# Kernel optimization log

Measured on AMD Instinct MI355X. Metric: run time of the kernel, lower is better.

The kernel has to match this reference:

```python
import jax, jax.numpy as jnp
import numpy as np

N_NODES = 100000   # graph size N
DIM     = 128      # embedding dim d
M_SEL   = 4096     # selected nodes per forward
N_POS   = 32       # positives per node (padded/fixed sample of pos_neigh)
N_NEG   = 256      # negatives per node (fixed sample of neg_samples)


def setup_inputs() -> dict:
    key = jax.random.key(0)
    ks = jax.random.split(key, 8)
    return {
        "P": jax.random.normal(ks[0], (N_NODES, DIM), dtype=jnp.float32),
        "W_d": jax.random.normal(ks[1], (DIM,), dtype=jnp.float32),
        "deg_vec": jax.random.uniform(ks[2], (N_NODES,), dtype=jnp.float32) * 64.0,
        "nodes": jax.random.randint(ks[3], (M_SEL,), 0, N_NODES),
        "pos_idx": jax.random.randint(ks[4], (M_SEL, N_POS), 0, N_NODES),
        "neg_idx": jax.random.randint(ks[5], (M_SEL, N_NEG), 0, N_NODES),
        "deg_pos_idx": jax.random.randint(ks[6], (M_SEL, N_POS), 0, N_NODES),
        "deg_neg_idx": jax.random.randint(ks[7], (M_SEL, N_NEG), 0, N_NODES),
    }


def my_sigmoid(x):
    # Sigmoid_alt: sign-carrying sigmoid in (-1, 1) (parity used in the repo's plots)
    return 2.0 * jax.nn.sigmoid(x) - 1.0


def _contrast(Z, nodes, pos_idx, neg_idx):
    # softmax_formula vectorized over the selected-node batch:
    #   loss_i = -( mean_p hamming(Z_i, Z_p) - log sum_n exp(hamming(Z_i, Z_n)) )
    Zi = Z[nodes]                                            # [M, d]
    h_pos = jnp.abs(Zi[:, None, :] - Z[pos_idx]).sum(-1)    # [M, P]
    h_neg = jnp.abs(Zi[:, None, :] - Z[neg_idx]).sum(-1)    # [M, K]
    log_sum_neg = jax.scipy.special.logsumexp(h_neg, axis=1)  # stable log(sum(exp(.)))
    per_node = log_sum_neg - h_pos.mean(axis=1)
    return per_node.sum()


def reference(P, W_d, deg_vec, nodes, pos_idx, neg_idx, deg_pos_idx, deg_neg_idx):
    Z = my_sigmoid(P)                                        # [N, d]
    # degree_loss: MSE(Z @ W_d, deg_vec)
    L_deg = jnp.mean((Z @ W_d - deg_vec) ** 2)
    # contrast_adj_n_degDist: adjacency and degree-distribution contrastive totals
    L_adj = _contrast(Z, nodes, pos_idx, neg_idx)
    L_deg_dist = _contrast(Z, nodes, deg_pos_idx, deg_neg_idx)
    return (L_adj, L_deg_dist, L_deg)
```

## Files before the change

kernel.cpp:

```cpp
#include <hip/hip_runtime.h>
#include <math.h>

#define N_NODES_C 100000
#define DIM_C     128
#define M_SEL_C   4096
#define N_POS_C   32
#define N_NEG_C   256
#define QS4       (2.0f / 15.0f)

__device__ __forceinline__ float wsum64(float v) {
#pragma unroll
    for (int o = 32; o; o >>= 1) v += __shfl_xor(v, o, 64);
    return v;
}
__device__ __forceinline__ float hsum32(float v) {
#pragma unroll
    for (int o = 1; o < 32; o <<= 1) v += __shfl_xor(v, o, 64);
    return v;
}
__device__ __forceinline__ int gsum4(int v) {
    v += __shfl_xor(v, 1, 64);
    v += __shfl_xor(v, 2, 64);
    return v;
}

__device__ __forceinline__ unsigned sad8(unsigned a, unsigned b, unsigned acc) {
    unsigned d;
    asm volatile("v_sad_u8 %0, %1, %2, %3" : "=v"(d) : "v"(a), "v"(b), "v"(acc));
    return d;
}

__device__ __forceinline__ int sadrow4(uint4 b, const unsigned* cl, const unsigned* ch) {
    const unsigned M = 0x0F0F0F0Fu;
    unsigned s = 0;
    s = sad8(b.x & M, cl[0], s); s = sad8((b.x >> 4) & M, ch[0], s);
    s = sad8(b.y & M, cl[1], s); s = sad8((b.y >> 4) & M, ch[1], s);
    s = sad8(b.z & M, cl[2], s); s = sad8((b.z >> 4) & M, ch[2], s);
    s = sad8(b.w & M, cl[3], s); s = sad8((b.w >> 4) & M, ch[3], s);
    return (int)s;
}

__global__ __launch_bounds__(256) void k_z_deg(
    const float* __restrict__ P, const float* __restrict__ Wd,
    const float* __restrict__ deg, unsigned short* __restrict__ Qh,
    float* __restrict__ out)
{
    const int lane = threadIdx.x & 63;
    const int sl   = lane & 31;
    const int hi   = lane >> 5;
    const int wv   = threadIdx.x >> 6;
    const int gw   = blockIdx.x * 4 + wv;
    const int nw   = gridDim.x * 4;
    const float4 w = *(const float4*)(Wd + 4 * sl);
    float acc = 0.0f;
    for (int pr = gw; pr < N_NODES_C / 2; pr += nw) {
        const int row = 2 * pr + hi;
        float4 p = *(const float4*)(P + (size_t)row * DIM_C + 4 * sl);
        float r0 = __fdividef(15.0f, 1.0f + __expf(-p.x));
        float r1 = __fdividef(15.0f, 1.0f + __expf(-p.y));
        float r2 = __fdividef(15.0f, 1.0f + __expf(-p.z));
        float r3 = __fdividef(15.0f, 1.0f + __expf(-p.w));
        unsigned q = __float2uint_rn(r0) | (__float2uint_rn(r1) << 4) |
                     (__float2uint_rn(r2) << 8) | (__float2uint_rn(r3) << 12);
        Qh[(size_t)row * (DIM_C / 4) + sl] = (unsigned short)q;
        float z0 = fmaf(r0, QS4, -1.0f), z1 = fmaf(r1, QS4, -1.0f);
        float z2 = fmaf(r2, QS4, -1.0f), z3 = fmaf(r3, QS4, -1.0f);
        float d4 = fmaf(z0, w.x, fmaf(z1, w.y, fmaf(z2, w.z, z3 * w.w)));
        d4 = hsum32(d4);
        if (sl == 0) { float d = d4 - deg[row]; acc = fmaf(d, d, acc); }
    }
    __shared__ float part[4];
    float a = wsum64(acc);
    if (lane == 0) part[wv] = a;
    __syncthreads();
    if (threadIdx.x == 0)
        atomicAdd(out + 2, (part[0] + part[1] + part[2] + part[3]) * (1.0f / N_NODES_C));
}

__global__ __launch_bounds__(256, 6) void k_contrast(
    const uint4* __restrict__ Q4,
    const int* __restrict__ nodes,
    const int* __restrict__ pos_a, const int* __restrict__ neg_a,
    const int* __restrict__ pos_b, const int* __restrict__ neg_b,
    float* __restrict__ out)
{
    const int tid  = threadIdx.x;
    const int wv   = tid >> 6;
    const int lane = tid & 63;
    const int l4   = lane & 3;
    const int g    = lane >> 2;

    const int id   = blockIdx.x * 4 + wv;
    const int sel  = id >> 12;
    const int m    = id & (M_SEL_C - 1);
    const int* __restrict__ pos_idx = sel ? pos_b : pos_a;
    const int* __restrict__ neg_idx = sel ? neg_b : neg_a;

    __shared__ int sNeg[4][N_NEG_C];
    __shared__ int sPos[4][N_POS_C];

    ((int4*)sNeg[wv])[lane] = ((const int4*)(neg_idx + m * N_NEG_C))[lane];
    if (lane < N_POS_C / 4)
        ((int4*)sPos[wv])[lane] = ((const int4*)(pos_idx + m * N_POS_C))[lane];
    const int node = nodes[m];
    uint4 c = Q4[((unsigned)node << 2) + l4];
    const unsigned M = 0x0F0F0F0Fu;
    unsigned cl[4] = { c.x & M, c.y & M, c.z & M, c.w & M };
    unsigned ch[4] = { (c.x >> 4) & M, (c.y >> 4) & M, (c.z >> 4) & M, (c.w >> 4) & M };
    __syncthreads();

    int pn0 = sPos[wv][g], pn1 = sPos[wv][16 + g];
    uint4 pb0 = Q4[((unsigned)pn0 << 2) + l4];
    uint4 pb1 = Q4[((unsigned)pn1 << 2) + l4];
    int psi = sadrow4(pb0, cl, ch) + sadrow4(pb1, cl, ch);

    float mx = -1e30f, sm = 0.0f;
#pragma unroll 1
    for (int r = 0; r < 2; ++r) {
        int nn[8];
#pragma unroll
        for (int u = 0; u < 8; ++u) nn[u] = sNeg[wv][r * 128 + u * 16 + g];
        uint4 nb[8];
#pragma unroll
        for (int u = 0; u < 8; ++u) nb[u] = Q4[((unsigned)nn[u] << 2) + l4];
#pragma unroll
        for (int u = 0; u < 8; ++u) {
            int s = gsum4(sadrow4(nb[u], cl, ch));
            float v = (float)s * QS4;
            float nm = fmaxf(mx, v);
            sm = fmaf(sm, __expf(mx - nm), __expf(v - nm));
            mx = nm;
        }
    }

    float ps = (float)psi;
#pragma unroll
    for (int o = 1; o < 4; o <<= 1) ps += __shfl_xor(ps, o, 64);
#pragma unroll
    for (int o = 4; o < 64; o <<= 1) {
        float om = __shfl_xor(mx, o, 64);
        float os = __shfl_xor(sm, o, 64);
        float nm = fmaxf(mx, om);
        sm = fmaf(sm, __expf(mx - nm), os * __expf(om - nm));
        mx = nm;
        ps += __shfl_xor(ps, o, 64);
    }

    if (lane == 0) {
        float lse = mx + __logf(sm);
        float pm  = ps * QS4 * (1.0f / N_POS_C);
        atomicAdd(out + sel, lse - pm);
    }
}

extern "C" void kernel_launch(void* const* d_in, const int* in_sizes, int n_in,
                              void* d_out, int out_size, void* d_ws, size_t ws_size,
                              hipStream_t stream) {
    const float* P    = (const float*)d_in[0];
    const float* Wd   = (const float*)d_in[1];
    const float* deg  = (const float*)d_in[2];
    const int* nodes  = (const int*)d_in[3];
    const int* pos_i  = (const int*)d_in[4];
    const int* neg_i  = (const int*)d_in[5];
    const int* dpos_i = (const int*)d_in[6];
    const int* dneg_i = (const int*)d_in[7];
    float* out = (float*)d_out;
    unsigned short* Qh = (unsigned short*)d_ws;

    hipMemsetAsync(out, 0, (size_t)out_size * sizeof(float), stream);
    k_z_deg<<<2048, 256, 0, stream>>>(P, Wd, deg, Qh, out);
    k_contrast<<<2048, 256, 0, stream>>>(
        (const uint4*)Qh, nodes, pos_i, neg_i, dpos_i, dneg_i, out);
}
```

Baseline: 238.7 us.

## Split each contrast row across two waves and pipeline neighbor gathers

Each selected node's 256 negatives are now split between two wavefronts, which doubles the grid and raises the occupancy hint to 8. The partial logsumexp and positive sums of the two waves are merged through shared memory. Neighbor indices are read directly from global memory instead of being staged in LDS, and the gathered rows are loaded through a rolling 4-deep prefetch. The aim is more memory-level parallelism and latency hiding on the random gathers, at the cost of duplicate center-row loads, more blocks and an extra block barrier.

```diff
diff --git a/kernel.cpp b/kernel.cpp
--- a/kernel.cpp
+++ b/kernel.cpp
@@ -77,7 +77,7 @@
         atomicAdd(out + 2, (part[0] + part[1] + part[2] + part[3]) * (1.0f / N_NODES_C));
 }
 
-__global__ __launch_bounds__(256, 6) void k_contrast(
+__global__ __launch_bounds__(256, 8) void k_contrast(
     const uint4* __restrict__ Q4,
     const int* __restrict__ nodes,
     const int* __restrict__ pos_a, const int* __restrict__ neg_a,
@@ -91,49 +91,48 @@
     const int g    = lane >> 2;
 
     const int id   = blockIdx.x * 4 + wv;
-    const int sel  = id >> 12;
-    const int m    = id & (M_SEL_C - 1);
+    const int pr   = id >> 1;
+    const int half = id & 1;
+    const int sel  = pr >> 12;
+    const int m    = pr & (M_SEL_C - 1);
     const int* __restrict__ pos_idx = sel ? pos_b : pos_a;
     const int* __restrict__ neg_idx = sel ? neg_b : neg_a;
 
-    __shared__ int sNeg[4][N_NEG_C];
-    __shared__ int sPos[4][N_POS_C];
-
-    ((int4*)sNeg[wv])[lane] = ((const int4*)(neg_idx + m * N_NEG_C))[lane];
-    if (lane < N_POS_C / 4)
-        ((int4*)sPos[wv])[lane] = ((const int4*)(pos_idx + m * N_POS_C))[lane];
     const int node = nodes[m];
     uint4 c = Q4[((unsigned)node << 2) + l4];
     const unsigned M = 0x0F0F0F0Fu;
     unsigned cl[4] = { c.x & M, c.y & M, c.z & M, c.w & M };
     unsigned ch[4] = { (c.x >> 4) & M, (c.y >> 4) & M, (c.z >> 4) & M, (c.w >> 4) & M };
-    __syncthreads();
 
-    int pn0 = sPos[wv][g], pn1 = sPos[wv][16 + g];
-    uint4 pb0 = Q4[((unsigned)pn0 << 2) + l4];
-    uint4 pb1 = Q4[((unsigned)pn1 << 2) + l4];
-    int psi = sadrow4(pb0, cl, ch) + sadrow4(pb1, cl, ch);
+    const int* __restrict__ np = neg_idx + m * N_NEG_C + half * 128;
+    int nn[8];
+#pragma unroll
+    for (int t = 0; t < 8; ++t) nn[t] = np[t * 16 + g];
+
+    uint4 nb[4];
+#pragma unroll
+    for (int u = 0; u < 4; ++u) nb[u] = Q4[((unsigned)nn[u] << 2) + l4];
 
     float mx = -1e30f, sm = 0.0f;
-#pragma unroll 1
-    for (int r = 0; r < 2; ++r) {
-        int nn[8];
 #pragma unroll
-        for (int u = 0; u < 8; ++u) nn[u] = sNeg[wv][r * 128 + u * 16 + g];
-        uint4 nb[8];
-#pragma unroll
-        for (int u = 0; u < 8; ++u) nb[u] = Q4[((unsigned)nn[u] << 2) + l4];
-#pragma unroll
-        for (int u = 0; u < 8; ++u) {
-            int s = gsum4(sadrow4(nb[u], cl, ch));
-            float v = (float)s * QS4;
-            float nm = fmaxf(mx, v);
-            sm = fmaf(sm, __expf(mx - nm), __expf(v - nm));
-            mx = nm;
-        }
+    for (int t = 0; t < 8; ++t) {
+        int s = gsum4(sadrow4(nb[t & 3], cl, ch));
+        if (t < 4) nb[t & 3] = Q4[((unsigned)nn[t + 4] << 2) + l4];
+        float v = (float)s * QS4;
+        float nm = fmaxf(mx, v);
+        sm = fmaf(sm, __expf(mx - nm), __expf(v - nm));
+        mx = nm;
     }
 
-    float ps = (float)psi;
+    float ps = 0.0f;
+    if (half) {
+        const int* __restrict__ pq = pos_idx + m * N_POS_C;
+        int p0 = pq[g], p1 = pq[16 + g];
+        uint4 b0 = Q4[((unsigned)p0 << 2) + l4];
+        uint4 b1 = Q4[((unsigned)p1 << 2) + l4];
+        ps = (float)(sadrow4(b0, cl, ch) + sadrow4(b1, cl, ch));
+    }
+
 #pragma unroll
     for (int o = 1; o < 4; o <<= 1) ps += __shfl_xor(ps, o, 64);
 #pragma unroll
@@ -146,9 +145,16 @@
         ps += __shfl_xor(ps, o, 64);
     }
 
-    if (lane == 0) {
-        float lse = mx + __logf(sm);
-        float pm  = ps * QS4 * (1.0f / N_POS_C);
+    __shared__ float mrgM[4], mrgS[4], mrgP[4];
+    if (lane == 0) { mrgM[wv] = mx; mrgS[wv] = sm; mrgP[wv] = ps; }
+    __syncthreads();
+    if (!(wv & 1) && lane == 0) {
+        float m0 = mrgM[wv],     s0 = mrgS[wv];
+        float m1 = mrgM[wv + 1], s1 = mrgS[wv + 1];
+        float nm = fmaxf(m0, m1);
+        float st = fmaf(s0, __expf(m0 - nm), s1 * __expf(m1 - nm));
+        float lse = nm + __logf(st);
+        float pm  = (mrgP[wv] + mrgP[wv + 1]) * QS4 * (1.0f / N_POS_C);
         atomicAdd(out + sel, lse - pm);
     }
 }
@@ -169,6 +175,6 @@
 
     hipMemsetAsync(out, 0, (size_t)out_size * sizeof(float), stream);
     k_z_deg<<<2048, 256, 0, stream>>>(P, Wd, deg, Qh, out);
-    k_contrast<<<2048, 256, 0, stream>>>(
+    k_contrast<<<4096, 256, 0, stream>>>(
         (const uint4*)Qh, nodes, pos_i, neg_i, dpos_i, dneg_i, out);
 }
```

Result: no change. 237.8 us (-0.4%).
